# Performance work log

Hardware: AMD Instinct MI355X
Metric: run time of the kernel (lower is better)

## Reference

```python
import jax, jax.numpy as jnp
import numpy as np

B, I, H = 4096, 1024, 1024


def setup_inputs() -> dict:
    key = jax.random.key(0)
    ks = jax.random.split(key, 7)
    s = 0.1  # matches uniform(-0.1, 0.1) init scale loosely
    return {
        "input": jax.random.normal(ks[0], (B, I), jnp.float32),
        "h_t": jax.random.normal(ks[1], (B, H), jnp.float32),
        "c_t": jax.random.normal(ks[2], (B, H), jnp.float32),
        "w_i": jax.random.uniform(ks[3], (I, 4 * H), jnp.float32, -s, s),
        "w_h": jax.random.uniform(ks[4], (H, 4 * H), jnp.float32, -s, s),
        "b_i": jax.random.uniform(ks[5], (4 * H,), jnp.float32, -s, s),
        "b_h": jax.random.uniform(ks[6], (4 * H,), jnp.float32, -s, s),
    }


def reference(input, h_t, c_t, w_i, w_h, b_i, b_h):
    # ifgo: [B, 4H] = x @ w_i + h @ w_h + b_i + b_h
    ifgo = input @ w_i + h_t @ w_h + (b_i + b_h)
    i, f, g, o = jnp.split(ifgo, 4, axis=1)
    i = jax.nn.sigmoid(i)
    f = jax.nn.sigmoid(f)
    g = jnp.tanh(g)
    o = jax.nn.sigmoid(o)
    c_new = f * c_t + i * g
    h_new = o * jnp.tanh(c_new)
    return (h_new, c_new)
```

## Files before the change

### kernel.cpp

```cpp
#include <hip/hip_runtime.h>
#include <stdint.h>

typedef __attribute__((ext_vector_type(8))) short short8;
typedef __attribute__((ext_vector_type(4))) float floatx4;

__device__ inline unsigned short f2bf(float x) {
  union { float f; unsigned int u; } v; v.f = x;
  unsigned int r = v.u + 0x7FFFu + ((v.u >> 16) & 1u);
  return (unsigned short)(r >> 16);
}

__global__ void pack_all(const float* __restrict__ x, const float* __restrict__ h,
                         const float* __restrict__ wi, const float* __restrict__ wh,
                         unsigned short* __restrict__ A,
                         unsigned short* __restrict__ Wt) {
  int bid = blockIdx.x;
  int t = threadIdx.x;
  if (bid < 4096) {
    int idx = bid * 256 + t;
    int row = idx >> 8;
    int kc  = (idx & 255) << 3;
    const float* src = (kc < 1024) ? (x + (size_t)row * 1024 + kc)
                                   : (h + (size_t)row * 1024 + (kc - 1024));
    float4 a = ((const float4*)src)[0];
    float4 b = ((const float4*)src)[1];
    uint4 o;
    o.x = f2bf(a.x) | ((unsigned)f2bf(a.y) << 16);
    o.y = f2bf(a.z) | ((unsigned)f2bf(a.w) << 16);
    o.z = f2bf(b.x) | ((unsigned)f2bf(b.y) << 16);
    o.w = f2bf(b.z) | ((unsigned)f2bf(b.w) << 16);
    *(uint4*)(A + (size_t)row * 2048 + kc) = o;
  } else {
    __shared__ float tile[64][65];
    int b2 = bid - 4096;
    int kt = b2 & 31;
    int nt = b2 >> 5;
    int k0 = kt << 6, n0 = nt << 6;
    const float* src = (k0 < 1024) ? (wi + (size_t)k0 * 4096)
                                   : (wh + (size_t)(k0 - 1024) * 4096);
    int c4 = (t & 15) << 2, rr = t >> 4;
#pragma unroll
    for (int p = 0; p < 4; ++p) {
      int kk = rr + p * 16;
      float4 v = *(const float4*)(src + (size_t)kk * 4096 + n0 + c4);
      tile[kk][c4 + 0] = v.x; tile[kk][c4 + 1] = v.y;
      tile[kk][c4 + 2] = v.z; tile[kk][c4 + 3] = v.w;
    }
    __syncthreads();
    int k8 = (t & 7) << 3, nn = t >> 3;
#pragma unroll
    for (int p = 0; p < 2; ++p) {
      int n = n0 + nn + p * 32;
      int hh = n & 1023, g = n >> 10;
      int R = ((hh >> 5) << 7) + (((hh >> 4) & 1) << 6) + (g << 4) + (hh & 15);
      int nl = nn + p * 32;
      uint4 o;
      o.x = f2bf(tile[k8 + 0][nl]) | ((unsigned)f2bf(tile[k8 + 1][nl]) << 16);
      o.y = f2bf(tile[k8 + 2][nl]) | ((unsigned)f2bf(tile[k8 + 3][nl]) << 16);
      o.z = f2bf(tile[k8 + 4][nl]) | ((unsigned)f2bf(tile[k8 + 5][nl]) << 16);
      o.w = f2bf(tile[k8 + 6][nl]) | ((unsigned)f2bf(tile[k8 + 7][nl]) << 16);
      *(uint4*)(Wt + (size_t)R * 2048 + k0 + k8) = o;
    }
  }
}

__device__ inline void gl_lds16(const void* g, void* l) {
  __builtin_amdgcn_global_load_lds(
      (const __attribute__((address_space(1))) void*)g,
      (__attribute__((address_space(3))) void*)l, 16, 0, 0);
}

__device__ inline float sigm(float x)  { return 1.0f / (1.0f + __expf(-x)); }
__device__ inline float tanhx(float x) { return 2.0f / (1.0f + __expf(-2.0f * x)) - 1.0f; }

__global__ void __launch_bounds__(256, 3) gemm_lstm(
    const unsigned short* __restrict__ A,
    const unsigned short* __restrict__ Bt,
    const float* __restrict__ ct,
    const float* __restrict__ bi,
    const float* __restrict__ bh,
    float* __restrict__ out) {
  constexpr int K = 2048;
  __shared__ char AsB[128 * 128];
  __shared__ char BsB[128 * 128];
  const int tid  = threadIdx.x;
  const int lane = tid & 63;
  const int wave = tid >> 6;
  const int wm = wave >> 1, wn = wave & 1;

  const int bid = blockIdx.x;
  const int g  = bid & 7;
  const int s  = bid >> 3;
  const int bx = (g << 2) + (s & 3);
  const int by = ((s >> 4) << 2) + ((s >> 2) & 3);
  const int m0 = by << 7;
  const int n0 = bx << 7;
  const int h0 = bx << 5;

  const int er = (lane >> 4) << 2;
  const int ec = lane & 15;
  const int h  = h0 + (wn << 4) + ec;
  float bias[4];
#pragma unroll
  for (int j = 0; j < 4; ++j) bias[j] = bi[j * 1024 + h] + bh[j * 1024 + h];

  const int sr = tid >> 3;
  const int cs = ((tid & 7) ^ (sr & 7)) << 4;
  const unsigned voff = (unsigned)sr * 4096u + (unsigned)cs;
  const char* aBase = (const char*)A  + (size_t)m0 * 4096;
  const char* bBase = (const char*)Bt + (size_t)n0 * 4096;
  char* aD = AsB + tid * 16;
  char* bD = BsB + tid * 16;

  floatx4 acc[4][4] = {};
  const int rA = (wm << 6) + (lane & 15);
  const int rB = (wn << 6) + (lane & 15);
  const int keyc = lane & 7;
  const int kq   = lane >> 4;
  const char* aF0 = AsB + rA * 128 + ((kq ^ keyc) << 4);
  const char* aF1 = AsB + rA * 128 + (((4 + kq) ^ keyc) << 4);
  const char* bF0 = BsB + rB * 128 + ((kq ^ keyc) << 4);
  const char* bF1 = BsB + rB * 128 + (((4 + kq) ^ keyc) << 4);

  for (int ks = 0; ks < K; ks += 64) {
    const char* aIt = aBase + ks * 2;
    const char* bIt = bBase + ks * 2;
#pragma unroll
    for (int p = 0; p < 4; ++p) gl_lds16(aIt + p * 131072 + voff, aD + p * 4096);
#pragma unroll
    for (int p = 0; p < 4; ++p) gl_lds16(bIt + p * 131072 + voff, bD + p * 4096);
    __syncthreads();
    {
      short8 af[4], bfr[4];
#pragma unroll
      for (int f = 0; f < 4; ++f) {
        af[f]  = *(const short8*)(aF0 + f * 2048);
        bfr[f] = *(const short8*)(bF0 + f * 2048);
      }
#pragma unroll
      for (int i = 0; i < 4; ++i)
#pragma unroll
        for (int j = 0; j < 4; ++j)
          acc[i][j] = __builtin_amdgcn_mfma_f32_16x16x32_bf16(af[i], bfr[j], acc[i][j], 0, 0, 0);
    }
    {
      short8 af[4], bfr[4];
#pragma unroll
      for (int f = 0; f < 4; ++f) {
        af[f]  = *(const short8*)(aF1 + f * 2048);
        bfr[f] = *(const short8*)(bF1 + f * 2048);
      }
#pragma unroll
      for (int i = 0; i < 4; ++i)
#pragma unroll
        for (int j = 0; j < 4; ++j)
          acc[i][j] = __builtin_amdgcn_mfma_f32_16x16x32_bf16(af[i], bfr[j], acc[i][j], 0, 0, 0);
    }
    __syncthreads();
  }

  float cv[4][4];
#pragma unroll
  for (int i = 0; i < 4; ++i)
#pragma unroll
    for (int rg = 0; rg < 4; ++rg) {
      int row = m0 + (wm << 6) + i * 16 + er + rg;
      cv[i][rg] = ct[(size_t)row * 1024 + h];
    }
#pragma unroll
  for (int i = 0; i < 4; ++i) {
#pragma unroll
    for (int rg = 0; rg < 4; ++rg) {
      int row = m0 + (wm << 6) + i * 16 + er + rg;
      size_t o = (size_t)row * 1024 + h;
      float iv = sigm(acc[i][0][rg] + bias[0]);
      float fv = sigm(acc[i][1][rg] + bias[1]);
      float gv = tanhx(acc[i][2][rg] + bias[2]);
      float ov = sigm(acc[i][3][rg] + bias[3]);
      float cn = fv * cv[i][rg] + iv * gv;
      out[o] = ov * tanhx(cn);
      out[4194304 + o] = cn;
    }
  }
}

extern "C" void kernel_launch(void* const* d_in, const int* in_sizes, int n_in,
                              void* d_out, int out_size, void* d_ws, size_t ws_size,
                              hipStream_t stream) {
  const float* x  = (const float*)d_in[0];
  const float* ht = (const float*)d_in[1];
  const float* ct = (const float*)d_in[2];
  const float* wi = (const float*)d_in[3];
  const float* wh = (const float*)d_in[4];
  const float* bi = (const float*)d_in[5];
  const float* bh = (const float*)d_in[6];
  float* out = (float*)d_out;

  char* ws = (char*)d_ws;
  unsigned short* Abf = (unsigned short*)ws;
  unsigned short* Wbf = (unsigned short*)(ws + (16u << 20));

  pack_all<<<6144, 256, 0, stream>>>(x, ht, wi, wh, Abf, Wbf);
  gemm_lstm<<<1024, 256, 0, stream>>>(Abf, Wbf, ct, bi, bh, out);
}
```

Before: 199.9 us.

## Use 256x256 tiles with double-buffered LDS pipeline and 8-wave blocks

```diff
diff --git a/kernel.cpp b/kernel.cpp
--- a/kernel.cpp
+++ b/kernel.cpp
@@ -73,105 +73,154 @@
 __device__ inline float sigm(float x)  { return 1.0f / (1.0f + __expf(-x)); }
 __device__ inline float tanhx(float x) { return 2.0f / (1.0f + __expf(-2.0f * x)) - 1.0f; }
 
-__global__ void __launch_bounds__(256, 3) gemm_lstm(
+#define MFMA_BF16 __builtin_amdgcn_mfma_f32_16x16x32_bf16
+
+#define STAGE(SRC, DST)                                              \
+  do {                                                               \
+    gl_lds16((SRC) + rOff, (DST) + tid * 16);                        \
+    gl_lds16((SRC) + rOff + (size_t)64 * 4096,                       \
+             (DST) + tid * 16 + 8192);                               \
+  } while (0)
+
+#define PHASE(I0, STAGE_STMT, TAIL_STMT)                                      \
+  {                                                                           \
+    short8 a0k0 = *(const short8*)(pa + (I0) * 2048 + c0);                    \
+    short8 a1k0 = *(const short8*)(pa + ((I0) + 1) * 2048 + c0);              \
+    short8 a0k1 = *(const short8*)(pa + (I0) * 2048 + c1);                    \
+    short8 a1k1 = *(const short8*)(pa + ((I0) + 1) * 2048 + c1);              \
+    STAGE_STMT;                                                               \
+    __builtin_amdgcn_s_barrier();                                             \
+    asm volatile("s_waitcnt lgkmcnt(0)" ::: "memory");                        \
+    __builtin_amdgcn_s_setprio(1);                                            \
+    _Pragma("unroll")                                                         \
+    for (int j = 0; j < 4; ++j) {                                             \
+      acc[(I0)][j]     = MFMA_BF16(a0k0, bf[j][0], acc[(I0)][j], 0, 0, 0);    \
+      acc[(I0) + 1][j] = MFMA_BF16(a1k0, bf[j][0], acc[(I0) + 1][j], 0, 0, 0);\
+    }                                                                         \
+    _Pragma("unroll")                                                         \
+    for (int j = 0; j < 4; ++j) {                                             \
+      acc[(I0)][j]     = MFMA_BF16(a0k1, bf[j][1], acc[(I0)][j], 0, 0, 0);    \
+      acc[(I0) + 1][j] = MFMA_BF16(a1k1, bf[j][1], acc[(I0) + 1][j], 0, 0, 0);\
+    }                                                                         \
+    __builtin_amdgcn_s_setprio(0);                                            \
+    TAIL_STMT;                                                                \
+    __builtin_amdgcn_s_barrier();                                             \
+  }
+
+__global__ void __launch_bounds__(512, 2) gemm_lstm(
     const unsigned short* __restrict__ A,
     const unsigned short* __restrict__ Bt,
     const float* __restrict__ ct,
     const float* __restrict__ bi,
     const float* __restrict__ bh,
     float* __restrict__ out) {
-  constexpr int K = 2048;
-  __shared__ char AsB[128 * 128];
-  __shared__ char BsB[128 * 128];
+  __shared__ __align__(16) char lds[131072];
+  char* Al = lds;
+  char* Bl = lds + 65536;
+
   const int tid  = threadIdx.x;
   const int lane = tid & 63;
   const int wave = tid >> 6;
-  const int wm = wave >> 1, wn = wave & 1;
+  const int wm = wave >> 2;
+  const int wn = wave & 3;
 
   const int bid = blockIdx.x;
-  const int g  = bid & 7;
-  const int s  = bid >> 3;
-  const int bx = (g << 2) + (s & 3);
-  const int by = ((s >> 4) << 2) + ((s >> 2) & 3);
-  const int m0 = by << 7;
-  const int n0 = bx << 7;
-  const int h0 = bx << 5;
+  const int gx = bid & 7;
+  const int sx = bid >> 3;
+  const int bx = (gx << 1) + (sx & 1);
+  const int by = sx >> 1;
+  const int m0 = by << 8;
+
+  const int ec = lane & 15;
+  const int h  = (bx << 6) + ((wn >> 1) << 5) + ((wn & 1) << 4) + ec;
+  float bias[4];
+#pragma unroll
+  for (int j = 0; j < 4; ++j) bias[j] = bi[j * 1024 + h] + bh[j * 1024 + h];
+
+  const int sr = tid >> 3;
+  const unsigned swz = (unsigned)(((tid & 7) ^ (sr & 7)) << 4);
+  const size_t rOff = (size_t)sr * 4096 + swz;
+  const char* aBase = (const char*)A  + (size_t)m0 * 4096;
+  const char* bBase = (const char*)Bt + (size_t)(bx << 8) * 4096;
+
+  const int lr  = lane & 15;
+  const int kq  = lane >> 4;
+  const int key = lane & 7;
+  const int c0  = (kq ^ key) << 4;
+  const int c1  = ((4 + kq) ^ key) << 4;
+  const int aRowOff = ((wm << 7) + lr) * 128;
+  const int bRowOff = ((wn << 6) + lr) * 128;
+
+  floatx4 acc[8][4] = {};
+
+  STAGE(bBase, Bl);
+  STAGE(bBase + (size_t)128 * 4096, Bl + 16384);
+  STAGE(aBase, Al);
+  STAGE(aBase + (size_t)128 * 4096, Al + 16384);
+  STAGE(bBase + 128, Bl + 32768);
+  STAGE(bBase + 128 + (size_t)128 * 4096, Bl + 32768 + 16384);
+  asm volatile("s_waitcnt vmcnt(4)" ::: "memory");
+  __builtin_amdgcn_s_barrier();
+
+  for (int t = 0; t < 32; ++t) {
+    const int buf = t & 1;
+    const char* cA = Al + (buf << 15);
+    const char* cB = Bl + (buf << 15);
+    char* nA = Al + ((buf ^ 1) << 15);
+    char* sB = Bl + (buf << 15);
+    const char* aSrc = aBase + (size_t)(((t + 1) & 31) << 7);
+    const char* bSrc = bBase + (size_t)(((t + 2) & 31) << 7);
+    const char* pa = cA + aRowOff;
+    const char* pb = cB + bRowOff;
+
+    short8 bf[4][2];
+    {
+#pragma unroll
+      for (int j = 0; j < 4; ++j) {
+        bf[j][0] = *(const short8*)(pb + j * 2048 + c0);
+        bf[j][1] = *(const short8*)(pb + j * 2048 + c1);
+      }
+      short8 a0k0 = *(const short8*)(pa + c0);
+      short8 a1k0 = *(const short8*)(pa + 2048 + c0);
+      short8 a0k1 = *(const short8*)(pa + c1);
+      short8 a1k1 = *(const short8*)(pa + 2048 + c1);
+      STAGE(aSrc, nA);
+      __builtin_amdgcn_s_barrier();
+      asm volatile("s_waitcnt lgkmcnt(0)" ::: "memory");
+      __builtin_amdgcn_s_setprio(1);
+#pragma unroll
+      for (int j = 0; j < 4; ++j) {
+        acc[0][j] = MFMA_BF16(a0k0, bf[j][0], acc[0][j], 0, 0, 0);
+        acc[1][j] = MFMA_BF16(a1k0, bf[j][0], acc[1][j], 0, 0, 0);
+      }
+#pragma unroll
+      for (int j = 0; j < 4; ++j) {
+        acc[0][j] = MFMA_BF16(a0k1, bf[j][1], acc[0][j], 0, 0, 0);
+        acc[1][j] = MFMA_BF16(a1k1, bf[j][1], acc[1][j], 0, 0, 0);
+      }
+      __builtin_amdgcn_s_setprio(0);
+      __builtin_amdgcn_s_barrier();
+    }
+    PHASE(2, STAGE(aSrc + (size_t)128 * 4096, nA + 16384), );
+    PHASE(4, STAGE(bSrc, sB), );
+    PHASE(6, STAGE(bSrc + (size_t)128 * 4096, sB + 16384),
+          asm volatile("s_waitcnt vmcnt(4)" ::: "memory"));
+  }
 
   const int er = (lane >> 4) << 2;
-  const int ec = lane & 15;
-  const int h  = h0 + (wn << 4) + ec;
-  float bias[4];
-#pragma unroll
-  for (int j = 0; j < 4; ++j) bias[j] = bi[j * 1024 + h] + bh[j * 1024 + h];
-
-  const int sr = tid >> 3;
-  const int cs = ((tid & 7) ^ (sr & 7)) << 4;
-  const unsigned voff = (unsigned)sr * 4096u + (unsigned)cs;
-  const char* aBase = (const char*)A  + (size_t)m0 * 4096;
-  const char* bBase = (const char*)Bt + (size_t)n0 * 4096;
-  char* aD = AsB + tid * 16;
-  char* bD = BsB + tid * 16;
-
-  floatx4 acc[4][4] = {};
-  const int rA = (wm << 6) + (lane & 15);
-  const int rB = (wn << 6) + (lane & 15);
-  const int keyc = lane & 7;
-  const int kq   = lane >> 4;
-  const char* aF0 = AsB + rA * 128 + ((kq ^ keyc) << 4);
-  const char* aF1 = AsB + rA * 128 + (((4 + kq) ^ keyc) << 4);
-  const char* bF0 = BsB + rB * 128 + ((kq ^ keyc) << 4);
-  const char* bF1 = BsB + rB * 128 + (((4 + kq) ^ keyc) << 4);
-
-  for (int ks = 0; ks < K; ks += 64) {
-    const char* aIt = aBase + ks * 2;
-    const char* bIt = bBase + ks * 2;
-#pragma unroll
-    for (int p = 0; p < 4; ++p) gl_lds16(aIt + p * 131072 + voff, aD + p * 4096);
-#pragma unroll
-    for (int p = 0; p < 4; ++p) gl_lds16(bIt + p * 131072 + voff, bD + p * 4096);
-    __syncthreads();
-    {
-      short8 af[4], bfr[4];
-#pragma unroll
-      for (int f = 0; f < 4; ++f) {
-        af[f]  = *(const short8*)(aF0 + f * 2048);
-        bfr[f] = *(const short8*)(bF0 + f * 2048);
-      }
-#pragma unroll
-      for (int i = 0; i < 4; ++i)
-#pragma unroll
-        for (int j = 0; j < 4; ++j)
-          acc[i][j] = __builtin_amdgcn_mfma_f32_16x16x32_bf16(af[i], bfr[j], acc[i][j], 0, 0, 0);
-    }
-    {
-      short8 af[4], bfr[4];
-#pragma unroll
-      for (int f = 0; f < 4; ++f) {
-        af[f]  = *(const short8*)(aF1 + f * 2048);
-        bfr[f] = *(const short8*)(bF1 + f * 2048);
-      }
-#pragma unroll
-      for (int i = 0; i < 4; ++i)
-#pragma unroll
-        for (int j = 0; j < 4; ++j)
-          acc[i][j] = __builtin_amdgcn_mfma_f32_16x16x32_bf16(af[i], bfr[j], acc[i][j], 0, 0, 0);
-    }
-    __syncthreads();
-  }
-
-  float cv[4][4];
-#pragma unroll
-  for (int i = 0; i < 4; ++i)
+  float cv[8][4];
+#pragma unroll
+  for (int i = 0; i < 8; ++i)
 #pragma unroll
     for (int rg = 0; rg < 4; ++rg) {
-      int row = m0 + (wm << 6) + i * 16 + er + rg;
+      int row = m0 + (wm << 7) + i * 16 + er + rg;
       cv[i][rg] = ct[(size_t)row * 1024 + h];
     }
 #pragma unroll
-  for (int i = 0; i < 4; ++i) {
+  for (int i = 0; i < 8; ++i) {
 #pragma unroll
     for (int rg = 0; rg < 4; ++rg) {
-      int row = m0 + (wm << 6) + i * 16 + er + rg;
+      int row = m0 + (wm << 7) + i * 16 + er + rg;
       size_t o = (size_t)row * 1024 + h;
       float iv = sigm(acc[i][0][rg] + bias[0]);
       float fv = sigm(acc[i][1][rg] + bias[1]);
@@ -201,5 +250,5 @@
   unsigned short* Wbf = (unsigned short*)(ws + (16u << 20));
 
   pack_all<<<6144, 256, 0, stream>>>(x, ht, wi, wh, Abf, Wbf);
-  gemm_lstm<<<1024, 256, 0, stream>>>(Abf, Wbf, ct, bi, bh, out);
-}
+  gemm_lstm<<<256, 512, 0, stream>>>(Abf, Wbf, ct, bi, bh, out);
+}
```

Result: faster. 194.3 us (-2.8%).
